# Optimization experiments

Hardware: AMD Instinct MI355X
Metric: run time of the kernel (lower is better)

Reference implementation:

```python
import jax, jax.numpy as jnp
import numpy as np

# (pt, eta, phi) feature indices per particle for each block (eta=None for MET)
A_PT, A_ETA, A_PHI = [5, 4, 35, 34], [9, 8, 45, 44], [13, 12, 55, 54]            # e3,e2,j9,j8
B_PT, B_ETA, B_PHI = [3, 33, 31, 2], [7, 43, 41, 6], [11, 53, 51, 10]            # e1,j7,j5,e0
C_PT, C_ETA, C_PHI = [28, 32, 15, 16], [38, 42, 19, 20], [48, 52, 23, 24]        # j2,j6,mu1,mu2
D_PT, D_ETA, D_PHI = [0, 14, 30, 26, 29, 27, 17], [None, 18, 40, 36, 39, 37, 21], [1, 22, 50, 46, 49, 47, 25]  # MET,mu0,j4,j0,j3,j1,mu3


def _bc(a, nd):
    # broadcast a (B,) or () angle factor over nd trailing qubit axes
    return a.reshape(a.shape + (1,) * nd)


def _rx(state, theta, w):
    nd = state.ndim - 2
    c = _bc(jnp.cos(theta * 0.5), nd)
    s = _bc(jnp.sin(theta * 0.5), nd)
    s0 = jnp.take(state, 0, axis=w + 1)
    s1 = jnp.take(state, 1, axis=w + 1)
    return jnp.stack([c * s0 - 1j * s * s1, -1j * s * s0 + c * s1], axis=w + 1)


def _ry(state, theta, w):
    nd = state.ndim - 2
    c = _bc(jnp.cos(theta * 0.5), nd)
    s = _bc(jnp.sin(theta * 0.5), nd)
    s0 = jnp.take(state, 0, axis=w + 1)
    s1 = jnp.take(state, 1, axis=w + 1)
    return jnp.stack([c * s0 - s * s1, s * s0 + c * s1], axis=w + 1)


def _rz(state, theta, w):
    nd = state.ndim - 2
    ph = _bc(jnp.exp(-0.5j * theta.astype(state.dtype)), nd)
    s0 = jnp.take(state, 0, axis=w + 1)
    s1 = jnp.take(state, 1, axis=w + 1)
    return jnp.stack([ph * s0, jnp.conj(ph) * s1], axis=w + 1)


def _cnot(state, ctrl, tgt):
    c0 = jnp.take(state, 0, axis=ctrl + 1)
    c1 = jnp.take(state, 1, axis=ctrl + 1)
    t_ax = tgt + 1 if tgt < ctrl else tgt  # ctrl axis removed shifts higher wires down
    c1 = jnp.flip(c1, axis=t_ax)
    return jnp.stack([c0, c1], axis=ctrl + 1)


def _extract(x, pt_idx, eta_idx, phi_idx):
    pt = x[:, np.array(pt_idx)]
    eta = jnp.stack([x[:, i] if i is not None else jnp.zeros(x.shape[0], x.dtype) for i in eta_idx], axis=1)
    phi = x[:, np.array(phi_idx)]
    return pt, eta, phi


def _run_block(pt, eta, phi, weights, n, latent, trash, depth):
    B = pt.shape[0]
    state = jnp.zeros((B,) + (2,) * n, dtype=jnp.complex64)
    state = state.at[(slice(None),) + (0,) * n].set(1.0)
    for k in range(n):
        state = _rx(state, eta[:, k], k)
        state = _ry(state, pt[:, k], k)
        state = _rz(state, phi[:, k], k)
    for k in range(n - 1):
        state = _cnot(state, k, k + 1)
    for k in range(n):
        state = _rz(state, eta[:, k], k)
        state = _ry(state, pt[:, k], k)
        state = _rx(state, phi[:, k], k)
    for d in range(depth):
        for t in trash:
            for l in latent:
                state = _cnot(state, t, l)
        for k in range(n):
            state = _ry(state, weights[d * n + k], k)
        for l in latent:
            for t in trash:
                state = _cnot(state, l, t)
    p = jnp.abs(state) ** 2  # (B, 2,...,2) real probabilities
    red = tuple(range(1, n))
    zs = [jnp.sum(jnp.take(p, 0, axis=w + 1), axis=red) - jnp.sum(jnp.take(p, 1, axis=w + 1), axis=red) for w in trash]
    return jnp.stack(zs, axis=1)


def setup_inputs() -> dict:
    key = jax.random.key(0)
    k0, k1, k2, k3, k4 = jax.random.split(key, 5)
    B = 131072
    x = jax.random.normal(k0, (B, 56), dtype=jnp.float32)
    wA = 0.01 * jax.random.normal(k1, (4,), dtype=jnp.float32)
    wB = 0.01 * jax.random.normal(k2, (4,), dtype=jnp.float32)
    wC = 0.01 * jax.random.normal(k3, (4,), dtype=jnp.float32)
    wD = 0.01 * jax.random.normal(k4, (28,), dtype=jnp.float32)
    return {"x": x, "wA": wA, "wB": wB, "wC": wC, "wD": wD}


def reference(x, wA, wB, wC, wD):
    zA = _run_block(*_extract(x, A_PT, A_ETA, A_PHI), wA, 4, (0, 1), (2, 3), 1)  # (B,2)
    zB = _run_block(*_extract(x, B_PT, B_ETA, B_PHI), wB, 4, (0, 1), (2, 3), 1)  # (B,2)
    zC = _run_block(*_extract(x, C_PT, C_ETA, C_PHI), wC, 4, (0, 1), (2, 3), 1)  # (B,2)
    zD = _run_block(*_extract(x, D_PT, D_ETA, D_PHI), wD, 7, (0, 1, 2, 3), (4, 5, 6), 4)  # (B,3)
    return jnp.concatenate([zA, zB, zC, zD], axis=1)  # (B,9) ~ dict values concatenated
```

## Files before the change

kernel.cpp:

```cpp
#include <hip/hip_runtime.h>
#include <hip/hip_fp16.h>


#define DEVINL __device__ __forceinline__

typedef _Float16 hv2 __attribute__((ext_vector_type(2)));

struct C2 { __half2 rr, mp; };

DEVINL C2 mkc(float re, float im) {
  C2 c; c.rr = __floats2half2_rn(re, re); c.mp = __floats2half2_rn(-im, im); return c;
}
DEVINL __half2 mkamp(float re, float im) { return __floats2half2_rn(re, im); }
DEVINL __half2 swap2(__half2 v) { return __lowhigh2highlow(v); }
DEVINL __half2 cmulc(C2 u, __half2 v) { return __hfma2(u.rr, v, __hmul2(u.mp, swap2(v))); }

DEVINL float ampsq(__half2 v, float acc) {
#if __has_builtin(__builtin_amdgcn_fdot2)
  return __builtin_amdgcn_fdot2(__builtin_bit_cast(hv2, v), __builtin_bit_cast(hv2, v), acc, false);
#else
  float2 f = __half22float2(v);
  return fmaf(f.x, f.x, fmaf(f.y, f.y, acc));
#endif
}

constexpr int parc(int x) { x ^= x >> 4; x ^= x >> 2; x ^= x >> 1; return x & 1; }

struct c32 { float x, y; };
DEVINL c32 cmulf(c32 a, c32 b) { return { a.x*b.x - a.y*b.y, a.x*b.y + a.y*b.x }; }


template<int N, int W>
DEVINL void g_ry(__half2* a, __half2 c2, __half2 s2, __half2 ns2) {
  constexpr int M = 1 << (N - 1 - W);
#pragma unroll
  for (int i = 0; i < (1 << N); ++i) if (!(i & M)) {
    const int j = i | M;
    __half2 v0 = a[i], v1 = a[j];
    a[i] = __hfma2(c2, v0, __hmul2(ns2, v1));
    a[j] = __hfma2(c2, v1, __hmul2(s2, v0));
  }
}

template<int N, int W>
DEVINL void g_u2(__half2* a, C2 u00, C2 u01, C2 u10, C2 u11) {
  constexpr int M = 1 << (N - 1 - W);
#pragma unroll
  for (int i = 0; i < (1 << N); ++i) if (!(i & M)) {
    const int j = i | M;
    __half2 v0 = a[i], v1 = a[j], v0s = swap2(v0), v1s = swap2(v1);
    a[i] = __hfma2(u00.rr, v0, __hfma2(u00.mp, v0s, __hfma2(u01.rr, v1, __hmul2(u01.mp, v1s))));
    a[j] = __hfma2(u10.rr, v0, __hfma2(u10.mp, v0s, __hfma2(u11.rr, v1, __hmul2(u11.mp, v1s))));
  }
}

template<int N, int C, int T>
DEVINL void g_cnot(__half2* a) {
  constexpr int CM = 1 << (N - 1 - C), TM = 1 << (N - 1 - T);
#pragma unroll
  for (int i = 0; i < (1 << N); ++i) if ((i & CM) && !(i & TM)) {
    const int j = i | TM;
    __half2 t = a[i]; a[i] = a[j]; a[j] = t;
  }
}

template<int N, int K>
DEVINL void chain_cnot(__half2* a) {
  if constexpr (K < N - 1) { g_cnot<N, K, K + 1>(a); chain_cnot<N, K + 1>(a); }
}


DEVINL void mk_u01(float ce, float se, float cp, float sp, float cf, float sf,
                   c32& u0, c32& u1) {
  u0 = cmulf({cf, -sf}, {cp * ce, sp * se});
  u1 = cmulf({cf,  sf}, {sp * ce, -cp * se});
}

DEVINL void mk_U(float ce, float se, float cp, float sp, float cf, float sf,
                 C2& U00, C2& U01, C2& U10, C2& U11) {
  c32 z = {ce, -se}, zb = {ce, se};
  c32 A = cmulf({cf * cp, -sf * sp}, z);
  c32 T = cmulf({cf * sp,  sf * cp}, zb);
  c32 Cc = cmulf({cf * sp, -sf * cp}, z);
  c32 D = cmulf({cf * cp,  sf * sp}, zb);
  U00 = mkc(A.x, A.y); U01 = mkc(-T.x, -T.y); U10 = mkc(Cc.x, Cc.y); U11 = mkc(D.x, D.y);
}

template<int N, int M>
DEVINL void build_step(__half2* a, const float* ce, const float* se, const float* cp,
                       const float* sp, const float* cf, const float* sf) {
  if constexpr (M < N) {
    c32 u0, u1; mk_u01(ce[M], se[M], cp[M], sp[M], cf[M], sf[M], u0, u1);
    C2 c0 = mkc(u0.x, u0.y), c1 = mkc(u1.x, u1.y);
#pragma unroll
    for (int j = (1 << M) - 1; j >= 0; --j) {
      __half2 s = a[j];
      a[2 * j]     = cmulc(c0, s);
      a[2 * j + 1] = cmulc(c1, s);
    }
    build_step<N, M + 1>(a, ce, se, cp, sp, cf, sf);
  }
}

template<int N, int K>
DEVINL void u_sweep(__half2* a, const float* ce, const float* se, const float* cp,
                    const float* sp, const float* cf, const float* sf) {
  if constexpr (K < N) {
    C2 U00, U01, U10, U11;
    mk_U(ce[K], se[K], cp[K], sp[K], cf[K], sf[K], U00, U01, U10, U11);
    g_u2<N, K>(a, U00, U01, U10, U11);
    u_sweep<N, K + 1>(a, ce, se, cp, sp, cf, sf);
  }
}

template<int N, int K>
DEVINL void ry_sweep(__half2* a, const __half2* c2, const __half2* s2, const __half2* ns2) {
  if constexpr (K < N) {
    g_ry<N, K>(a, c2[K], s2[K], ns2[K]);
    ry_sweep<N, K + 1>(a, c2, s2, ns2);
  }
}


template<int I>
DEVINL void sim4h(const float* r, const float* __restrict__ w, float* z) {
  constexpr int PT[3][4]  = {{5, 4, 35, 34}, {3, 33, 31, 2}, {28, 32, 15, 16}};
  constexpr int ETA[3][4] = {{9, 8, 45, 44}, {7, 43, 41, 6}, {38, 42, 19, 20}};
  constexpr int PHI[3][4] = {{13, 12, 55, 54}, {11, 53, 51, 10}, {48, 52, 23, 24}};
  float ce[4], se[4], cp[4], sp[4], cf[4], sf[4];
#pragma unroll
  for (int k = 0; k < 4; ++k) {
    __sincosf(0.5f * r[ETA[I][k]], &se[k], &ce[k]);
    __sincosf(0.5f * r[PT[I][k]],  &sp[k], &cp[k]);
    __sincosf(0.5f * r[PHI[I][k]], &sf[k], &cf[k]);
  }
  __half2 a[16];
  a[0] = mkamp(1.f, 0.f);
  build_step<4, 0>(a, ce, se, cp, sp, cf, sf);
  chain_cnot<4, 0>(a);
  u_sweep<4, 0>(a, ce, se, cp, sp, cf, sf);

#pragma unroll
  for (int i = 0; i < 16; ++i)
    if (parc(i & 3) && !(i & 8)) { __half2 t = a[i]; a[i] = a[i ^ 12]; a[i ^ 12] = t; }

  __half2 c2[4], s2[4], ns2[4];
#pragma unroll
  for (int k = 0; k < 4; ++k) {
    float sv, cv; __sincosf(0.5f * w[k], &sv, &cv);
    c2[k] = __floats2half2_rn(cv, cv);
    s2[k] = __floats2half2_rn(sv, sv);
    ns2[k] = __floats2half2_rn(-sv, -sv);
  }
  ry_sweep<4, 0>(a, c2, s2, ns2);

#pragma unroll
  for (int i = 0; i < 16; ++i)
    if (parc(i & 12) && !(i & 2)) { __half2 t = a[i]; a[i] = a[i ^ 3]; a[i ^ 3] = t; }

  float cls[4] = {0.f, 0.f, 0.f, 0.f};
#pragma unroll
  for (int i = 0; i < 16; ++i) cls[i & 3] = ampsq(a[i], cls[i & 3]);
  float z0 = 0.f, z1 = 0.f;
#pragma unroll
  for (int c = 0; c < 4; ++c) {
    z0 += (c & 2) ? -cls[c] : cls[c];
    z1 += (c & 1) ? -cls[c] : cls[c];
  }
  z[0] = z0; z[1] = z1;
}


DEVINL void sim7h(const float* r, const float* __restrict__ wD, float* z) {
  constexpr int PT[7]  = {0, 14, 30, 26, 29, 27, 17};
  constexpr int ETA[7] = {-1, 18, 40, 36, 39, 37, 21};
  constexpr int PHI[7] = {1, 22, 50, 46, 49, 47, 25};
  float ce[7], se[7], cp[7], sp[7], cf[7], sf[7];
#pragma unroll
  for (int k = 0; k < 7; ++k) {
    float e = (ETA[k] < 0) ? 0.f : r[ETA[k]];
    __sincosf(0.5f * e, &se[k], &ce[k]);
    __sincosf(0.5f * r[PT[k]],  &sp[k], &cp[k]);
    __sincosf(0.5f * r[PHI[k]], &sf[k], &cf[k]);
  }
  __half2 a[128];
  a[0] = mkamp(1.f, 0.f);
  build_step<7, 0>(a, ce, se, cp, sp, cf, sf);
  chain_cnot<7, 0>(a);
  u_sweep<7, 0>(a, ce, se, cp, sp, cf, sf);

#pragma unroll
  for (int d = 0; d < 4; ++d) {
#pragma unroll
    for (int i = 0; i < 128; ++i)
      if (parc(i & 7) && !(i & 64)) { __half2 t = a[i]; a[i] = a[i ^ 0x78]; a[i ^ 0x78] = t; }

    __half2 c2[7], s2[7], ns2[7];
#pragma unroll
    for (int k = 0; k < 7; ++k) {
      float sv, cv; __sincosf(0.5f * wD[d * 7 + k], &sv, &cv);
      c2[k] = __floats2half2_rn(cv, cv);
      s2[k] = __floats2half2_rn(sv, sv);
      ns2[k] = __floats2half2_rn(-sv, -sv);
    }
    ry_sweep<7, 0>(a, c2, s2, ns2);

#pragma unroll
    for (int i = 0; i < 128; ++i)
      if (parc(i & 0x78) && !(i & 4)) { __half2 t = a[i]; a[i] = a[i ^ 7]; a[i ^ 7] = t; }
  }

  float cls[8] = {0.f, 0.f, 0.f, 0.f, 0.f, 0.f, 0.f, 0.f};
#pragma unroll
  for (int i = 0; i < 128; ++i) cls[i & 7] = ampsq(a[i], cls[i & 7]);
  float z4 = 0.f, z5 = 0.f, z6 = 0.f;
#pragma unroll
  for (int c = 0; c < 8; ++c) {
    z4 += (c & 4) ? -cls[c] : cls[c];
    z5 += (c & 2) ? -cls[c] : cls[c];
    z6 += (c & 1) ? -cls[c] : cls[c];
  }
  z[0] = z4; z[1] = z5; z[2] = z6;
}


__global__ void __launch_bounds__(256, 1)
k_all(const float* __restrict__ x,
      const float* __restrict__ wA, const float* __restrict__ wB,
      const float* __restrict__ wC, const float* __restrict__ wD,
      float* __restrict__ out, int B) {
  const int b = blockIdx.x * blockDim.x + threadIdx.x;
  if (b >= B) return;

  float r[56];
  const float4* row4 = (const float4*)(x + (size_t)b * 56);
#pragma unroll
  for (int i = 0; i < 14; ++i) {
    float4 v = row4[i];
    r[4 * i] = v.x; r[4 * i + 1] = v.y; r[4 * i + 2] = v.z; r[4 * i + 3] = v.w;
  }

  float* op = out + (size_t)b * 9;

  float o[6];
  sim4h<0>(r, wA, &o[0]);
  sim4h<1>(r, wB, &o[2]);
  sim4h<2>(r, wC, &o[4]);
#pragma unroll
  for (int i = 0; i < 6; ++i) op[i] = o[i];

  float z[3];
  sim7h(r, wD, z);
  op[6] = z[0]; op[7] = z[1]; op[8] = z[2];
}


extern "C" void kernel_launch(void* const* d_in, const int* in_sizes, int n_in,
                              void* d_out, int out_size, void* d_ws, size_t ws_size,
                              hipStream_t stream) {
  const float* x  = (const float*)d_in[0];
  const float* wA = (const float*)d_in[1];
  const float* wB = (const float*)d_in[2];
  const float* wC = (const float*)d_in[3];
  const float* wD = (const float*)d_in[4];
  float* out = (float*)d_out;
  const int B = in_sizes[0] / 56;
  const int threads = 256;
  const int grid = (B + threads - 1) / threads;
  k_all<<<grid, threads, 0, stream>>>(x, wA, wB, wC, wD, out, B);
}
```

Baseline: 139.1 us.

## Precompute weight trig in a prologue kernel and cut per-thread register and ALU work

Adds a tiny kernel that computes the half-precision cos/sin pairs for all 40 trainable weights once into workspace, so the main kernel loads them instead of doing per-thread sincos. The two-qubit unitary now uses two complex coefficients (A, C) via the SU(2) structure instead of four, reducing constants and FMAs. The depth loop in the 7-qubit block is no longer unrolled and launch bounds ask for two blocks per CU, aiming to lower register pressure and code size. Risks are an extra kernel launch, global loads of weights inside the hot loop, and possible spilling of the 128-element state under the tighter register budget.

```diff
diff --git a/kernel.cpp b/kernel.cpp
--- a/kernel.cpp
+++ b/kernel.cpp
@@ -1,28 +1,29 @@
 #include <hip/hip_runtime.h>
-#include <hip/hip_fp16.h>
 
 
 #define DEVINL __device__ __forceinline__
 
-typedef _Float16 hv2 __attribute__((ext_vector_type(2)));
-
-struct C2 { __half2 rr, mp; };
-
-DEVINL C2 mkc(float re, float im) {
-  C2 c; c.rr = __floats2half2_rn(re, re); c.mp = __floats2half2_rn(-im, im); return c;
-}
-DEVINL __half2 mkamp(float re, float im) { return __floats2half2_rn(re, im); }
-DEVINL __half2 swap2(__half2 v) { return __lowhigh2highlow(v); }
-DEVINL __half2 cmulc(C2 u, __half2 v) { return __hfma2(u.rr, v, __hmul2(u.mp, swap2(v))); }
-
-DEVINL float ampsq(__half2 v, float acc) {
+typedef _Float16 h2 __attribute__((ext_vector_type(2)));
+
+DEVINL h2 hswap(h2 v) { return __builtin_shufflevector(v, v, 1, 0); }
+DEVINL h2 ffma(h2 a, h2 b, h2 c) { return __builtin_elementwise_fma(a, b, c); }
+DEVINL h2 cvt2(float a, float b) {
+  h2 r; r.x = (_Float16)a; r.y = (_Float16)b; return r;
+}
+DEVINL h2 uash2(unsigned u) { return __builtin_bit_cast(h2, u); }
+
+DEVINL float ampsq(h2 v, float acc) {
 #if __has_builtin(__builtin_amdgcn_fdot2)
-  return __builtin_amdgcn_fdot2(__builtin_bit_cast(hv2, v), __builtin_bit_cast(hv2, v), acc, false);
+  return __builtin_amdgcn_fdot2(v, v, acc, false);
 #else
-  float2 f = __half22float2(v);
-  return fmaf(f.x, f.x, fmaf(f.y, f.y, acc));
+  float x = (float)v.x, y = (float)v.y;
+  return fmaf(x, x, fmaf(y, y, acc));
 #endif
 }
+
+struct CC { h2 rr, mp; };
+DEVINL CC mkcc(float re, float im) { return { cvt2(re, re), cvt2(-im, im) }; }
+DEVINL h2 cmulc(CC u, h2 v) { return ffma(u.rr, v, u.mp * hswap(v)); }
 
 constexpr int parc(int x) { x ^= x >> 4; x ^= x >> 2; x ^= x >> 1; return x & 1; }
 
@@ -31,41 +32,42 @@
 
 
 template<int N, int W>
-DEVINL void g_ry(__half2* a, __half2 c2, __half2 s2, __half2 ns2) {
+DEVINL void g_ry(h2* a, h2 c2, h2 s2) {
   constexpr int M = 1 << (N - 1 - W);
 #pragma unroll
   for (int i = 0; i < (1 << N); ++i) if (!(i & M)) {
     const int j = i | M;
-    __half2 v0 = a[i], v1 = a[j];
-    a[i] = __hfma2(c2, v0, __hmul2(ns2, v1));
-    a[j] = __hfma2(c2, v1, __hmul2(s2, v0));
+    h2 v0 = a[i], v1 = a[j];
+    a[i] = ffma(c2, v0, -(s2 * v1));
+    a[j] = ffma(s2, v0, c2 * v1);
   }
 }
 
 template<int N, int W>
-DEVINL void g_u2(__half2* a, C2 u00, C2 u01, C2 u10, C2 u11) {
+DEVINL void g_u2(h2* a, h2 Arr, h2 Amp, h2 Crr, h2 Cmp) {
   constexpr int M = 1 << (N - 1 - W);
 #pragma unroll
   for (int i = 0; i < (1 << N); ++i) if (!(i & M)) {
     const int j = i | M;
-    __half2 v0 = a[i], v1 = a[j], v0s = swap2(v0), v1s = swap2(v1);
-    a[i] = __hfma2(u00.rr, v0, __hfma2(u00.mp, v0s, __hfma2(u01.rr, v1, __hmul2(u01.mp, v1s))));
-    a[j] = __hfma2(u10.rr, v0, __hfma2(u10.mp, v0s, __hfma2(u11.rr, v1, __hmul2(u11.mp, v1s))));
+    h2 v0 = a[i], v1 = a[j], s0 = hswap(v0), s1 = hswap(v1);
+    h2 o0 = Arr * v0; o0 = ffma(Amp, s0, o0); o0 = ffma(Cmp, s1, o0); o0 = ffma(-Crr, v1, o0);
+    h2 o1 = Crr * v0; o1 = ffma(Cmp, s0, o1); o1 = ffma(-Amp, s1, o1); o1 = ffma(Arr, v1, o1);
+    a[i] = o0; a[j] = o1;
   }
 }
 
 template<int N, int C, int T>
-DEVINL void g_cnot(__half2* a) {
+DEVINL void g_cnot(h2* a) {
   constexpr int CM = 1 << (N - 1 - C), TM = 1 << (N - 1 - T);
 #pragma unroll
   for (int i = 0; i < (1 << N); ++i) if ((i & CM) && !(i & TM)) {
     const int j = i | TM;
-    __half2 t = a[i]; a[i] = a[j]; a[j] = t;
+    h2 t = a[i]; a[i] = a[j]; a[j] = t;
   }
 }
 
 template<int N, int K>
-DEVINL void chain_cnot(__half2* a) {
+DEVINL void chain_cnot(h2* a) {
   if constexpr (K < N - 1) { g_cnot<N, K, K + 1>(a); chain_cnot<N, K + 1>(a); }
 }
 
@@ -76,25 +78,22 @@
   u1 = cmulf({cf,  sf}, {sp * ce, -cp * se});
 }
 
-DEVINL void mk_U(float ce, float se, float cp, float sp, float cf, float sf,
-                 C2& U00, C2& U01, C2& U10, C2& U11) {
-  c32 z = {ce, -se}, zb = {ce, se};
-  c32 A = cmulf({cf * cp, -sf * sp}, z);
-  c32 T = cmulf({cf * sp,  sf * cp}, zb);
-  c32 Cc = cmulf({cf * sp, -sf * cp}, z);
-  c32 D = cmulf({cf * cp,  sf * sp}, zb);
-  U00 = mkc(A.x, A.y); U01 = mkc(-T.x, -T.y); U10 = mkc(Cc.x, Cc.y); U11 = mkc(D.x, D.y);
+DEVINL void mk_AC(float ce, float se, float cp, float sp, float cf, float sf,
+                  c32& A, c32& C) {
+  c32 z = {ce, -se};
+  A = cmulf({cf * cp, -sf * sp}, z);
+  C = cmulf({cf * sp, -sf * cp}, z);
 }
 
 template<int N, int M>
-DEVINL void build_step(__half2* a, const float* ce, const float* se, const float* cp,
+DEVINL void build_step(h2* a, const float* ce, const float* se, const float* cp,
                        const float* sp, const float* cf, const float* sf) {
   if constexpr (M < N) {
     c32 u0, u1; mk_u01(ce[M], se[M], cp[M], sp[M], cf[M], sf[M], u0, u1);
-    C2 c0 = mkc(u0.x, u0.y), c1 = mkc(u1.x, u1.y);
+    CC c0 = mkcc(u0.x, u0.y), c1 = mkcc(u1.x, u1.y);
 #pragma unroll
     for (int j = (1 << M) - 1; j >= 0; --j) {
-      __half2 s = a[j];
+      h2 s = a[j];
       a[2 * j]     = cmulc(c0, s);
       a[2 * j + 1] = cmulc(c1, s);
     }
@@ -103,27 +102,28 @@
 }
 
 template<int N, int K>
-DEVINL void u_sweep(__half2* a, const float* ce, const float* se, const float* cp,
+DEVINL void u_sweep(h2* a, const float* ce, const float* se, const float* cp,
                     const float* sp, const float* cf, const float* sf) {
   if constexpr (K < N) {
-    C2 U00, U01, U10, U11;
-    mk_U(ce[K], se[K], cp[K], sp[K], cf[K], sf[K], U00, U01, U10, U11);
-    g_u2<N, K>(a, U00, U01, U10, U11);
+    c32 A, C;
+    mk_AC(ce[K], se[K], cp[K], sp[K], cf[K], sf[K], A, C);
+    g_u2<N, K>(a, cvt2(A.x, A.x), cvt2(-A.y, A.y), cvt2(C.x, C.x), cvt2(-C.y, C.y));
     u_sweep<N, K + 1>(a, ce, se, cp, sp, cf, sf);
   }
 }
 
 template<int N, int K>
-DEVINL void ry_sweep(__half2* a, const __half2* c2, const __half2* s2, const __half2* ns2) {
+DEVINL void ry_sweep_wt(h2* a, const uint2* __restrict__ w) {
   if constexpr (K < N) {
-    g_ry<N, K>(a, c2[K], s2[K], ns2[K]);
-    ry_sweep<N, K + 1>(a, c2, s2, ns2);
+    uint2 q = w[K];
+    g_ry<N, K>(a, uash2(q.x), uash2(q.y));
+    ry_sweep_wt<N, K + 1>(a, w);
   }
 }
 
 
 template<int I>
-DEVINL void sim4h(const float* r, const float* __restrict__ w, float* z) {
+DEVINL void sim4h(const float* r, const uint2* __restrict__ wt, float* z) {
   constexpr int PT[3][4]  = {{5, 4, 35, 34}, {3, 33, 31, 2}, {28, 32, 15, 16}};
   constexpr int ETA[3][4] = {{9, 8, 45, 44}, {7, 43, 41, 6}, {38, 42, 19, 20}};
   constexpr int PHI[3][4] = {{13, 12, 55, 54}, {11, 53, 51, 10}, {48, 52, 23, 24}};
@@ -134,29 +134,21 @@
     __sincosf(0.5f * r[PT[I][k]],  &sp[k], &cp[k]);
     __sincosf(0.5f * r[PHI[I][k]], &sf[k], &cf[k]);
   }
-  __half2 a[16];
-  a[0] = mkamp(1.f, 0.f);
+  h2 a[16];
+  a[0] = cvt2(1.f, 0.f);
   build_step<4, 0>(a, ce, se, cp, sp, cf, sf);
   chain_cnot<4, 0>(a);
   u_sweep<4, 0>(a, ce, se, cp, sp, cf, sf);
 
 #pragma unroll
   for (int i = 0; i < 16; ++i)
-    if (parc(i & 3) && !(i & 8)) { __half2 t = a[i]; a[i] = a[i ^ 12]; a[i ^ 12] = t; }
-
-  __half2 c2[4], s2[4], ns2[4];
-#pragma unroll
-  for (int k = 0; k < 4; ++k) {
-    float sv, cv; __sincosf(0.5f * w[k], &sv, &cv);
-    c2[k] = __floats2half2_rn(cv, cv);
-    s2[k] = __floats2half2_rn(sv, sv);
-    ns2[k] = __floats2half2_rn(-sv, -sv);
-  }
-  ry_sweep<4, 0>(a, c2, s2, ns2);
+    if (parc(i & 3) && !(i & 8)) { h2 t = a[i]; a[i] = a[i ^ 12]; a[i ^ 12] = t; }
+
+  ry_sweep_wt<4, 0>(a, wt + 4 * I);
 
 #pragma unroll
   for (int i = 0; i < 16; ++i)
-    if (parc(i & 12) && !(i & 2)) { __half2 t = a[i]; a[i] = a[i ^ 3]; a[i ^ 3] = t; }
+    if (parc(i & 12) && !(i & 2)) { h2 t = a[i]; a[i] = a[i ^ 3]; a[i ^ 3] = t; }
 
   float cls[4] = {0.f, 0.f, 0.f, 0.f};
 #pragma unroll
@@ -171,7 +163,7 @@
 }
 
 
-DEVINL void sim7h(const float* r, const float* __restrict__ wD, float* z) {
+DEVINL void sim7h(const float* r, const uint2* __restrict__ wtD, float* z) {
   constexpr int PT[7]  = {0, 14, 30, 26, 29, 27, 17};
   constexpr int ETA[7] = {-1, 18, 40, 36, 39, 37, 21};
   constexpr int PHI[7] = {1, 22, 50, 46, 49, 47, 25};
@@ -183,31 +175,23 @@
     __sincosf(0.5f * r[PT[k]],  &sp[k], &cp[k]);
     __sincosf(0.5f * r[PHI[k]], &sf[k], &cf[k]);
   }
-  __half2 a[128];
-  a[0] = mkamp(1.f, 0.f);
+  h2 a[128];
+  a[0] = cvt2(1.f, 0.f);
   build_step<7, 0>(a, ce, se, cp, sp, cf, sf);
   chain_cnot<7, 0>(a);
   u_sweep<7, 0>(a, ce, se, cp, sp, cf, sf);
 
-#pragma unroll
+#pragma unroll 1
   for (int d = 0; d < 4; ++d) {
 #pragma unroll
     for (int i = 0; i < 128; ++i)
-      if (parc(i & 7) && !(i & 64)) { __half2 t = a[i]; a[i] = a[i ^ 0x78]; a[i ^ 0x78] = t; }
-
-    __half2 c2[7], s2[7], ns2[7];
-#pragma unroll
-    for (int k = 0; k < 7; ++k) {
-      float sv, cv; __sincosf(0.5f * wD[d * 7 + k], &sv, &cv);
-      c2[k] = __floats2half2_rn(cv, cv);
-      s2[k] = __floats2half2_rn(sv, sv);
-      ns2[k] = __floats2half2_rn(-sv, -sv);
-    }
-    ry_sweep<7, 0>(a, c2, s2, ns2);
+      if (parc(i & 7) && !(i & 64)) { h2 t = a[i]; a[i] = a[i ^ 0x78]; a[i ^ 0x78] = t; }
+
+    ry_sweep_wt<7, 0>(a, wtD + d * 7);
 
 #pragma unroll
     for (int i = 0; i < 128; ++i)
-      if (parc(i & 0x78) && !(i & 4)) { __half2 t = a[i]; a[i] = a[i ^ 7]; a[i ^ 7] = t; }
+      if (parc(i & 0x78) && !(i & 4)) { h2 t = a[i]; a[i] = a[i ^ 7]; a[i ^ 7] = t; }
   }
 
   float cls[8] = {0.f, 0.f, 0.f, 0.f, 0.f, 0.f, 0.f, 0.f};
@@ -224,10 +208,19 @@
 }
 
 
-__global__ void __launch_bounds__(256, 1)
-k_all(const float* __restrict__ x,
-      const float* __restrict__ wA, const float* __restrict__ wB,
-      const float* __restrict__ wC, const float* __restrict__ wD,
+__global__ void k_wt(const float* __restrict__ wA, const float* __restrict__ wB,
+                     const float* __restrict__ wC, const float* __restrict__ wD,
+                     uint2* __restrict__ wt) {
+  const int t = threadIdx.x;
+  if (t >= 40) return;
+  float w = (t < 4) ? wA[t] : (t < 8) ? wB[t - 4] : (t < 12) ? wC[t - 8] : wD[t - 12];
+  float sv, cv; __sincosf(0.5f * w, &sv, &cv);
+  wt[t] = make_uint2(__builtin_bit_cast(unsigned, cvt2(cv, cv)),
+                     __builtin_bit_cast(unsigned, cvt2(sv, sv)));
+}
+
+__global__ void __launch_bounds__(256, 2)
+k_all(const float* __restrict__ x, const uint2* __restrict__ wt,
       float* __restrict__ out, int B) {
   const int b = blockIdx.x * blockDim.x + threadIdx.x;
   if (b >= B) return;
@@ -243,14 +236,14 @@
   float* op = out + (size_t)b * 9;
 
   float o[6];
-  sim4h<0>(r, wA, &o[0]);
-  sim4h<1>(r, wB, &o[2]);
-  sim4h<2>(r, wC, &o[4]);
+  sim4h<0>(r, wt, &o[0]);
+  sim4h<1>(r, wt, &o[2]);
+  sim4h<2>(r, wt, &o[4]);
 #pragma unroll
   for (int i = 0; i < 6; ++i) op[i] = o[i];
 
   float z[3];
-  sim7h(r, wD, z);
+  sim7h(r, wt + 12, z);
   op[6] = z[0]; op[7] = z[1]; op[8] = z[2];
 }
 
@@ -264,8 +257,10 @@
   const float* wC = (const float*)d_in[3];
   const float* wD = (const float*)d_in[4];
   float* out = (float*)d_out;
+  uint2* wt = (uint2*)d_ws;
   const int B = in_sizes[0] / 56;
   const int threads = 256;
   const int grid = (B + threads - 1) / threads;
-  k_all<<<grid, threads, 0, stream>>>(x, wA, wB, wC, wD, out, B);
-}
+  k_wt<<<1, 64, 0, stream>>>(wA, wB, wC, wD, wt);
+  k_all<<<grid, threads, 0, stream>>>(x, wt, out, B);
+}
```

After: 128.8 us. 1.08x faster.
